# Performance work log

Measured on AMD Instinct MI355X. Metric: run time of the kernel, lower is better.

## Reference

```python
import jax, jax.numpy as jnp
import numpy as np

B, S, F, H, W = 16, 2048, 512, 512, 5
PAD = W // 2


def setup_inputs() -> dict:
    key = jax.random.key(0)
    k = jax.random.split(key, 6)
    scale = 0.02
    return {
        "embeds_output": jax.random.normal(k[0], (B, S, F), dtype=jnp.float32),
        "Wq": jax.random.normal(k[1], (F, H), dtype=jnp.float32) * scale,
        "Wk": jax.random.normal(k[2], (F, H), dtype=jnp.float32) * scale,
        "v_att": jax.random.normal(k[3], (H,), dtype=jnp.float32) * scale,
        "cnn_W": jax.random.normal(k[4], (W * F, H), dtype=jnp.float32) * scale,
        "cnn_b": jax.random.normal(k[5], (H,), dtype=jnp.float32) * scale,
    }


def reference(embeds_output, Wq, Wk, v_att, cnn_W, cnn_b):
    b, s, f = embeds_output.shape
    # getConvEmbeds: zero-pad and gather W shifted views -> [B, S, W, F]
    xp = jnp.pad(embeds_output, ((0, 0), (PAD, PAD), (0, 0)))
    windows = jnp.stack([xp[:, i:i + s, :] for i in range(W)], axis=2)  # [B,S,W,F]
    entity = windows[:, :, PAD, :]  # center token, [B,S,F]
    # Bahdanau additive attention over the window
    q = jnp.einsum('bsf,fh->bsh', entity, Wq)          # [B,S,H]
    kproj = jnp.einsum('bswf,fh->bswh', windows, Wk)   # [B,S,W,H]
    scores = jnp.einsum('bswh,h->bsw', jnp.tanh(kproj + q[:, :, None, :]), v_att)
    att = jax.nn.softmax(scores, axis=-1)              # [B,S,W]
    # weight contexts, flatten window dim (row-major W*F, matching torch reshape)
    att_context = (att[..., None] * windows).reshape(b, s, W * F)
    return att_context @ cnn_W + cnn_b                 # [B,S,H]
```

## Files before the change

kernel.cpp:

```cpp
#include <hip/hip_runtime.h>
#include <stdint.h>
#include <stddef.h>

typedef unsigned short u16;
typedef __attribute__((ext_vector_type(8))) short s16x8;
typedef __attribute__((ext_vector_type(8))) unsigned short u16x8;
typedef __attribute__((ext_vector_type(4))) unsigned short u16x4;
typedef __attribute__((ext_vector_type(4))) float f32x4;

typedef __attribute__((address_space(3))) void* as3_void_p;
typedef const __attribute__((address_space(1))) void* as1_cvoid_p;

#define GLD16(gp, lp) __builtin_amdgcn_global_load_lds((as1_cvoid_p)(gp), (as3_void_p)(lp), 16, 0, 0)

enum {
  NS = 2048, NF = 512, NH = 512, NW = 5,
  NROW = 32768,
  K2 = NW * NF,
  XBLOCKS = NROW * NF / 4 / 256,
  W_ELEMS = 1024 * 512 + 512 * K2,
  WBLOCKS = (W_ELEMS + 255) / 256
};

__device__ __forceinline__ u16 f2bf(float f) {
  unsigned u = __float_as_uint(f);
  u += 0x7FFFu + ((u >> 16) & 1u);
  return (u16)(u >> 16);
}
__device__ __forceinline__ float bf2f(u16 v) {
  return __uint_as_float(((unsigned)v) << 16);
}


__global__ __launch_bounds__(256) void cvt_all(const float* __restrict__ X,
                                               const float* __restrict__ Wq,
                                               const float* __restrict__ Wk,
                                               const float* __restrict__ cnnW,
                                               u16* __restrict__ Xb,
                                               u16* __restrict__ Wt1,
                                               u16* __restrict__ Wt2) {
  int b = blockIdx.x;
  if (b < XBLOCKS) {
    int i = b * 256 + threadIdx.x;
    f32x4 v = ((const f32x4*)X)[i];
    u16x4 o;
    o.x = f2bf(v.x); o.y = f2bf(v.y); o.z = f2bf(v.z); o.w = f2bf(v.w);
    ((u16x4*)Xb)[i] = o;
  } else {
    int i = (b - XBLOCKS) * 256 + threadIdx.x;
    if (i >= W_ELEMS) return;
    if (i < 1024 * 512) {
      int j = i >> 9, f = i & 511;
      float v = (j < 512) ? Wq[(size_t)f * 512 + j] : Wk[(size_t)f * 512 + (j - 512)];
      Wt1[i] = f2bf(v);
    } else {
      int t = i - 1024 * 512;
      int h = t / K2, k = t % K2;
      Wt2[t] = f2bf(cnnW[(size_t)k * 512 + h]);
    }
  }
}


__global__ __launch_bounds__(512, 4) void gemm_qk(const u16* __restrict__ Xb,
                                                  const u16* __restrict__ Wt1,
                                                  u16* __restrict__ QKb) {
  __shared__ u16 As[128 * 64];
  __shared__ u16 Bs[128 * 64];
  const int tid  = threadIdx.x;
  const int lane = tid & 63, wid = tid >> 6;
  const int wr = wid >> 2, wc = wid & 3;
  const int fr = lane & 15, fq = lane >> 4;
  const int wgid = (blockIdx.x & 7) * 256 + (blockIdx.x >> 3);
  const int brow = (wgid >> 3) * 128;
  const int bcol = (wgid & 7) * 128;

  const int rsub = tid >> 3;
  const int cb   = (((tid & 7) ^ (rsub & 7)) << 4);
  const char* gA0 = (const char*)(Xb  + (size_t)(brow + rsub) * NF) + cb;
  const char* gA1 = (const char*)(Xb  + (size_t)(brow + 64 + rsub) * NF) + cb;
  const char* gB0 = (const char*)(Wt1 + (size_t)(bcol + rsub) * NF) + cb;
  const char* gB1 = (const char*)(Wt1 + (size_t)(bcol + 64 + rsub) * NF) + cb;

  f32x4 acc[4][2] = {};

  for (int kt = 0; kt < 8; ++kt) {
    const int ko = kt * 128;
    GLD16(gA0 + ko, (char*)As + tid * 16);
    GLD16(gA1 + ko, (char*)As + 8192 + tid * 16);
    GLD16(gB0 + ko, (char*)Bs + tid * 16);
    GLD16(gB1 + ko, (char*)Bs + 8192 + tid * 16);
    __syncthreads();
#pragma unroll
    for (int kk = 0; kk < 2; ++kk) {
      s16x8 af[4], bfr[2];
#pragma unroll
      for (int m = 0; m < 4; ++m) {
        int row = wr * 64 + m * 16 + fr;
        af[m] = *(const s16x8*)((const char*)As + row * 128 + ((kk * 64 + fq * 16) ^ ((row & 7) << 4)));
      }
#pragma unroll
      for (int n = 0; n < 2; ++n) {
        int row = wc * 32 + n * 16 + fr;
        bfr[n] = *(const s16x8*)((const char*)Bs + row * 128 + ((kk * 64 + fq * 16) ^ ((row & 7) << 4)));
      }
#pragma unroll
      for (int m = 0; m < 4; ++m)
#pragma unroll
        for (int n = 0; n < 2; ++n)
          acc[m][n] = __builtin_amdgcn_mfma_f32_16x16x32_bf16(af[m], bfr[n], acc[m][n], 0, 0, 0);
    }
    __syncthreads();
  }

#pragma unroll
  for (int m = 0; m < 4; ++m)
#pragma unroll
    for (int n = 0; n < 2; ++n)
#pragma unroll
      for (int r = 0; r < 4; ++r) {
        int row = brow + wr * 64 + m * 16 + fq * 4 + r;
        int col = bcol + wc * 32 + n * 16 + fr;
        QKb[(size_t)row * 1024 + col] = f2bf(acc[m][n][r]);
      }
}


__global__ __launch_bounds__(256) void scores_att(const u16* __restrict__ QKb,
                                                  const float* __restrict__ vatt,
                                                  float* __restrict__ att) {
  const int lane = threadIdx.x & 63;
  const int wid  = threadIdx.x >> 6;
  const int wgid = (blockIdx.x & 7) * 1024 + (blockIdx.x >> 3);
  const int n = wgid * 4 + wid;
  const int s = n & (NS - 1);
  const int h0 = lane * 8;

  u16x8 qv = *(const u16x8*)(QKb + (size_t)n * 1024 + h0);
  f32x4 va0 = *(const f32x4*)(vatt + h0);
  f32x4 va1 = *(const f32x4*)(vatt + h0 + 4);
  float q[8], vv[8];
#pragma unroll
  for (int j = 0; j < 8; ++j) q[j] = bf2f(qv[j]);
  vv[0] = va0.x; vv[1] = va0.y; vv[2] = va0.z; vv[3] = va0.w;
  vv[4] = va1.x; vv[5] = va1.y; vv[6] = va1.z; vv[7] = va1.w;

  float sc[5];
#pragma unroll
  for (int w = 0; w < 5; ++w) {
    int sp = s + w - 2;
    u16x8 kv = {0, 0, 0, 0, 0, 0, 0, 0};
    if (sp >= 0 && sp < NS)
      kv = *(const u16x8*)(QKb + (size_t)(n + w - 2) * 1024 + 512 + h0);
    float acc = 0.f;
#pragma unroll
    for (int j = 0; j < 8; ++j) {
      float x = q[j] + bf2f(kv[j]);
      x = fminf(fmaxf(x, -15.f), 15.f);
      float e = __expf(2.f * x);
      acc += vv[j] * ((e - 1.f) / (e + 1.f));
    }
    sc[w] = acc;
  }
#pragma unroll
  for (int w = 0; w < 5; ++w)
#pragma unroll
    for (int o = 32; o > 0; o >>= 1)
      sc[w] += __shfl_xor(sc[w], o, 64);

  if (lane == 0) {
    float m = sc[0];
#pragma unroll
    for (int w = 1; w < 5; ++w) m = fmaxf(m, sc[w]);
    float e[5], sum = 0.f;
#pragma unroll
    for (int w = 0; w < 5; ++w) { e[w] = __expf(sc[w] - m); sum += e[w]; }
    float inv = 1.f / sum;
#pragma unroll
    for (int w = 0; w < 5; ++w) att[(size_t)n * 5 + w] = e[w] * inv;
  }
}


__global__ __launch_bounds__(512, 4) void gemm_out(const u16* __restrict__ Xb,
                                                   const u16* __restrict__ Wt2,
                                                   const float* __restrict__ att,
                                                   const float* __restrict__ cnnb,
                                                   float* __restrict__ out) {
  __shared__ u16 As[128 * 64];
  __shared__ u16 Bs[128 * 64];
  __shared__ float att_s[128 * 5];
  const int tid  = threadIdx.x;
  const int lane = tid & 63, wid = tid >> 6;
  const int wr = wid >> 2, wc = wid & 3;
  const int fr = lane & 15, fq = lane >> 4;
  const int wgid = (blockIdx.x & 7) * 128 + (blockIdx.x >> 3);
  const int brow = (wgid >> 2) * 128;
  const int bcol = (wgid & 3) * 128;

  if (tid < 128) {
    int s = (brow + tid) & (NS - 1);
#pragma unroll
    for (int w = 0; w < 5; ++w) {
      int sp = s + w - 2;
      att_s[tid * 5 + w] = (sp >= 0 && sp < NS) ? att[(size_t)(brow + tid) * 5 + w] : 0.f;
    }
  }

  const int rsub = tid >> 3;
  const int cb   = (((tid & 7) ^ (rsub & 7)) << 4);
  const char* gB0 = (const char*)(Wt2 + (size_t)(bcol + rsub) * K2) + cb;
  const char* gB1 = (const char*)(Wt2 + (size_t)(bcol + 64 + rsub) * K2) + cb;

  f32x4 acc[4][2] = {};
  f32x4 accOut[4][2] = {};

  for (int w = 0; w < 5; ++w) {
    int g0 = brow + rsub + w - 2;
    int g1 = brow + 64 + rsub + w - 2;
    g0 = g0 < 0 ? 0 : (g0 >= NROW ? NROW - 1 : g0);
    g1 = g1 < 0 ? 0 : (g1 >= NROW ? NROW - 1 : g1);
    const char* gA0 = (const char*)(Xb + (size_t)g0 * NF) + cb;
    const char* gA1 = (const char*)(Xb + (size_t)g1 * NF) + cb;
    const char* gBw0 = gB0 + w * 1024;
    const char* gBw1 = gB1 + w * 1024;

    for (int kt = 0; kt < 8; ++kt) {
      const int ko = kt * 128;
      GLD16(gA0  + ko, (char*)As + tid * 16);
      GLD16(gA1  + ko, (char*)As + 8192 + tid * 16);
      GLD16(gBw0 + ko, (char*)Bs + tid * 16);
      GLD16(gBw1 + ko, (char*)Bs + 8192 + tid * 16);
      __syncthreads();
#pragma unroll
      for (int kk = 0; kk < 2; ++kk) {
        s16x8 af[4], bfr[2];
#pragma unroll
        for (int m = 0; m < 4; ++m) {
          int row = wr * 64 + m * 16 + fr;
          af[m] = *(const s16x8*)((const char*)As + row * 128 + ((kk * 64 + fq * 16) ^ ((row & 7) << 4)));
        }
#pragma unroll
        for (int n = 0; n < 2; ++n) {
          int row = wc * 32 + n * 16 + fr;
          bfr[n] = *(const s16x8*)((const char*)Bs + row * 128 + ((kk * 64 + fq * 16) ^ ((row & 7) << 4)));
        }
#pragma unroll
        for (int m = 0; m < 4; ++m)
#pragma unroll
          for (int n = 0; n < 2; ++n)
            acc[m][n] = __builtin_amdgcn_mfma_f32_16x16x32_bf16(af[m], bfr[n], acc[m][n], 0, 0, 0);
      }
      __syncthreads();
    }
#pragma unroll
    for (int m = 0; m < 4; ++m) {
      float a0 = att_s[(wr * 64 + m * 16 + fq * 4 + 0) * 5 + w];
      float a1 = att_s[(wr * 64 + m * 16 + fq * 4 + 1) * 5 + w];
      float a2 = att_s[(wr * 64 + m * 16 + fq * 4 + 2) * 5 + w];
      float a3 = att_s[(wr * 64 + m * 16 + fq * 4 + 3) * 5 + w];
#pragma unroll
      for (int n = 0; n < 2; ++n) {
        accOut[m][n][0] += a0 * acc[m][n][0];
        accOut[m][n][1] += a1 * acc[m][n][1];
        accOut[m][n][2] += a2 * acc[m][n][2];
        accOut[m][n][3] += a3 * acc[m][n][3];
        acc[m][n] = f32x4{0.f, 0.f, 0.f, 0.f};
      }
    }
  }

#pragma unroll
  for (int m = 0; m < 4; ++m)
#pragma unroll
    for (int n = 0; n < 2; ++n)
#pragma unroll
      for (int r = 0; r < 4; ++r) {
        int row = brow + wr * 64 + m * 16 + fq * 4 + r;
        int col = bcol + wc * 32 + n * 16 + fr;
        out[(size_t)row * NH + col] = accOut[m][n][r] + cnnb[col];
      }
}


extern "C" void kernel_launch(void* const* d_in, const int* in_sizes, int n_in,
                              void* d_out, int out_size, void* d_ws, size_t ws_size,
                              hipStream_t stream) {
  const float* X    = (const float*)d_in[0];
  const float* Wq   = (const float*)d_in[1];
  const float* Wk   = (const float*)d_in[2];
  const float* vatt = (const float*)d_in[3];
  const float* cnnW = (const float*)d_in[4];
  const float* cnnb = (const float*)d_in[5];
  float* out = (float*)d_out;

  char* ws = (char*)d_ws;
  u16*   Xb  = (u16*)ws;
  u16*   Wt1 = (u16*)(ws + 33554432);
  u16*   Wt2 = (u16*)(ws + 34603008);
  u16*   QKb = (u16*)(ws + 37224448);
  float* att = (float*)(ws + 104333312);

  cvt_all<<<dim3(XBLOCKS + WBLOCKS), dim3(256), 0, stream>>>(X, Wq, Wk, cnnW, Xb, Wt1, Wt2);
  gemm_qk<<<dim3(2048), dim3(512), 0, stream>>>(Xb, Wt1, QKb);
  scores_att<<<dim3(NROW / 4), dim3(256), 0, stream>>>(QKb, vatt, att);
  gemm_out<<<dim3(1024), dim3(512), 0, stream>>>(Xb, Wt2, att, cnnb, out);
}
```

Before: 202.0 us.

## Double-buffer LDS tiles in gemm_out to overlap global loads with MFMA

Splits the A and B shared-memory tiles into two buffers and prefetches the next K-tile, or the first tile of the next window shift, with global_load_lds while the current tile feeds the MFMAs. Partial waits on vmcnt and raw s_barrier replace the full __syncthreads pairs, so load latency is meant to hide behind compute. LDS use doubles to about 64KB per block, which may lower occupancy under launch_bounds(512,4). The vmcnt counting is hand-managed, so it is fragile if the compiler emits other vector memory operations.

```diff
diff --git a/kernel.cpp b/kernel.cpp
--- a/kernel.cpp
+++ b/kernel.cpp
@@ -187,8 +187,8 @@
                                                    const float* __restrict__ att,
                                                    const float* __restrict__ cnnb,
                                                    float* __restrict__ out) {
-  __shared__ u16 As[128 * 64];
-  __shared__ u16 Bs[128 * 64];
+  __shared__ u16 As[2][128 * 64];
+  __shared__ u16 Bs[2][128 * 64];
   __shared__ float att_s[128 * 5];
   const int tid  = threadIdx.x;
   const int lane = tid & 63, wid = tid >> 6;
@@ -212,62 +212,98 @@
   const char* gB0 = (const char*)(Wt2 + (size_t)(bcol + rsub) * K2) + cb;
   const char* gB1 = (const char*)(Wt2 + (size_t)(bcol + 64 + rsub) * K2) + cb;
 
+  auto abase = [&](int w, int add64) -> const char* {
+    int g = brow + add64 + rsub + w - 2;
+    g = g < 0 ? 0 : (g >= NROW ? NROW - 1 : g);
+    return (const char*)(Xb + (size_t)g * NF) + cb;
+  };
+
   f32x4 acc[4][2] = {};
   f32x4 accOut[4][2] = {};
 
+  const char* gA0 = abase(0, 0);
+  const char* gA1 = abase(0, 64);
+
+  GLD16(gA0, (char*)As[0] + tid * 16);
+  GLD16(gA1, (char*)As[0] + 8192 + tid * 16);
+  GLD16(gB0, (char*)Bs[0] + tid * 16);
+  GLD16(gB1, (char*)Bs[0] + 8192 + tid * 16);
+  __syncthreads();
+
+  int cur = 0;
   for (int w = 0; w < 5; ++w) {
-    int g0 = brow + rsub + w - 2;
-    int g1 = brow + 64 + rsub + w - 2;
-    g0 = g0 < 0 ? 0 : (g0 >= NROW ? NROW - 1 : g0);
-    g1 = g1 < 0 ? 0 : (g1 >= NROW ? NROW - 1 : g1);
-    const char* gA0 = (const char*)(Xb + (size_t)g0 * NF) + cb;
-    const char* gA1 = (const char*)(Xb + (size_t)g1 * NF) + cb;
     const char* gBw0 = gB0 + w * 1024;
     const char* gBw1 = gB1 + w * 1024;
+    const char* nA0 = (w < 4) ? abase(w + 1, 0)  : gA0;
+    const char* nA1 = (w < 4) ? abase(w + 1, 64) : gA1;
 
     for (int kt = 0; kt < 8; ++kt) {
-      const int ko = kt * 128;
-      GLD16(gA0  + ko, (char*)As + tid * 16);
-      GLD16(gA1  + ko, (char*)As + 8192 + tid * 16);
-      GLD16(gBw0 + ko, (char*)Bs + tid * 16);
-      GLD16(gBw1 + ko, (char*)Bs + 8192 + tid * 16);
-      __syncthreads();
+      const bool last = (w == 4) && (kt == 7);
+      const int nb = cur ^ 1;
+      if (!last) {
+        if (kt < 7) {
+          const int ko = (kt + 1) * 128;
+          GLD16(gA0  + ko, (char*)As[nb] + tid * 16);
+          GLD16(gA1  + ko, (char*)As[nb] + 8192 + tid * 16);
+          GLD16(gBw0 + ko, (char*)Bs[nb] + tid * 16);
+          GLD16(gBw1 + ko, (char*)Bs[nb] + 8192 + tid * 16);
+        } else {
+          GLD16(nA0,         (char*)As[nb] + tid * 16);
+          GLD16(nA1,         (char*)As[nb] + 8192 + tid * 16);
+          GLD16(gBw0 + 1024, (char*)Bs[nb] + tid * 16);
+          GLD16(gBw1 + 1024, (char*)Bs[nb] + 8192 + tid * 16);
+        }
+        asm volatile("s_waitcnt vmcnt(4)" ::: "memory");
+      } else {
+        asm volatile("s_waitcnt vmcnt(0)" ::: "memory");
+      }
+      __builtin_amdgcn_s_barrier();
+
+      const char* Ab = (const char*)As[cur];
+      const char* Bb = (const char*)Bs[cur];
 #pragma unroll
       for (int kk = 0; kk < 2; ++kk) {
         s16x8 af[4], bfr[2];
 #pragma unroll
         for (int m = 0; m < 4; ++m) {
           int row = wr * 64 + m * 16 + fr;
-          af[m] = *(const s16x8*)((const char*)As + row * 128 + ((kk * 64 + fq * 16) ^ ((row & 7) << 4)));
+          af[m] = *(const s16x8*)(Ab + row * 128 + ((kk * 64 + fq * 16) ^ ((row & 7) << 4)));
         }
 #pragma unroll
         for (int n = 0; n < 2; ++n) {
           int row = wc * 32 + n * 16 + fr;
-          bfr[n] = *(const s16x8*)((const char*)Bs + row * 128 + ((kk * 64 + fq * 16) ^ ((row & 7) << 4)));
+          bfr[n] = *(const s16x8*)(Bb + row * 128 + ((kk * 64 + fq * 16) ^ ((row & 7) << 4)));
         }
+        asm volatile("s_waitcnt lgkmcnt(0)" ::: "memory");
+        __builtin_amdgcn_sched_barrier(0);
 #pragma unroll
         for (int m = 0; m < 4; ++m)
 #pragma unroll
           for (int n = 0; n < 2; ++n)
             acc[m][n] = __builtin_amdgcn_mfma_f32_16x16x32_bf16(af[m], bfr[n], acc[m][n], 0, 0, 0);
       }
-      __syncthreads();
-    }
-#pragma unroll
-    for (int m = 0; m < 4; ++m) {
-      float a0 = att_s[(wr * 64 + m * 16 + fq * 4 + 0) * 5 + w];
-      float a1 = att_s[(wr * 64 + m * 16 + fq * 4 + 1) * 5 + w];
-      float a2 = att_s[(wr * 64 + m * 16 + fq * 4 + 2) * 5 + w];
-      float a3 = att_s[(wr * 64 + m * 16 + fq * 4 + 3) * 5 + w];
-#pragma unroll
-      for (int n = 0; n < 2; ++n) {
-        accOut[m][n][0] += a0 * acc[m][n][0];
-        accOut[m][n][1] += a1 * acc[m][n][1];
-        accOut[m][n][2] += a2 * acc[m][n][2];
-        accOut[m][n][3] += a3 * acc[m][n][3];
-        acc[m][n] = f32x4{0.f, 0.f, 0.f, 0.f};
-      }
-    }
+      if (kt == 7) {
+#pragma unroll
+        for (int m = 0; m < 4; ++m) {
+          float a0 = att_s[(wr * 64 + m * 16 + fq * 4 + 0) * 5 + w];
+          float a1 = att_s[(wr * 64 + m * 16 + fq * 4 + 1) * 5 + w];
+          float a2 = att_s[(wr * 64 + m * 16 + fq * 4 + 2) * 5 + w];
+          float a3 = att_s[(wr * 64 + m * 16 + fq * 4 + 3) * 5 + w];
+#pragma unroll
+          for (int n = 0; n < 2; ++n) {
+            accOut[m][n][0] += a0 * acc[m][n][0];
+            accOut[m][n][1] += a1 * acc[m][n][1];
+            accOut[m][n][2] += a2 * acc[m][n][2];
+            accOut[m][n][3] += a3 * acc[m][n][3];
+            acc[m][n] = f32x4{0.f, 0.f, 0.f, 0.f};
+          }
+        }
+      }
+      __builtin_amdgcn_s_barrier();
+      cur ^= 1;
+    }
+    gA0 = nA0;
+    gA1 = nA1;
   }
 
 #pragma unroll
```

New measurement: 201.0 us. Within noise of the previous version (-0.5%).

## Triple-buffer LDS with async prefetch and enlarge GEMM row tiles to 256

Applied to the files above, without the earlier changes.

Both bf16 GEMMs move from single-buffered LDS with two syncthreads per K step to a three-slot ring buffer. Global-to-LDS loads are issued two stages ahead and gated by vmcnt waits plus one barrier per iteration. The output tile grows to 256 rows, which doubles A reuse per B fragment, and gemm_out flattens its window and K loops into one 40-step pipeline. The cost is more LDS (about 144KB per block), more accumulator registers, occupancy lowered to 2 blocks, and half as many blocks in the grid.

```diff
diff --git a/kernel.cpp b/kernel.cpp
--- a/kernel.cpp
+++ b/kernel.cpp
@@ -62,64 +62,82 @@
 }
 
 
-__global__ __launch_bounds__(512, 4) void gemm_qk(const u16* __restrict__ Xb,
+__global__ __launch_bounds__(512, 2) void gemm_qk(const u16* __restrict__ Xb,
                                                   const u16* __restrict__ Wt1,
                                                   u16* __restrict__ QKb) {
-  __shared__ u16 As[128 * 64];
-  __shared__ u16 Bs[128 * 64];
+  __shared__ u16 As[3][256 * 64];
+  __shared__ u16 Bs[3][128 * 64];
   const int tid  = threadIdx.x;
   const int lane = tid & 63, wid = tid >> 6;
   const int wr = wid >> 2, wc = wid & 3;
   const int fr = lane & 15, fq = lane >> 4;
-  const int wgid = (blockIdx.x & 7) * 256 + (blockIdx.x >> 3);
-  const int brow = (wgid >> 3) * 128;
+  const int wgid = (blockIdx.x & 7) * 128 + (blockIdx.x >> 3);
+  const int brow = (wgid >> 3) * 256;
   const int bcol = (wgid & 7) * 128;
 
   const int rsub = tid >> 3;
-  const int cb   = (((tid & 7) ^ (rsub & 7)) << 4);
-  const char* gA0 = (const char*)(Xb  + (size_t)(brow + rsub) * NF) + cb;
-  const char* gA1 = (const char*)(Xb  + (size_t)(brow + 64 + rsub) * NF) + cb;
-  const char* gB0 = (const char*)(Wt1 + (size_t)(bcol + rsub) * NF) + cb;
-  const char* gB1 = (const char*)(Wt1 + (size_t)(bcol + 64 + rsub) * NF) + cb;
-
-  f32x4 acc[4][2] = {};
-
-  for (int kt = 0; kt < 8; ++kt) {
-    const int ko = kt * 128;
-    GLD16(gA0 + ko, (char*)As + tid * 16);
-    GLD16(gA1 + ko, (char*)As + 8192 + tid * 16);
-    GLD16(gB0 + ko, (char*)Bs + tid * 16);
-    GLD16(gB1 + ko, (char*)Bs + 8192 + tid * 16);
-    __syncthreads();
+  const int cbyte = (((tid & 7) ^ (rsub & 7)) << 4);
+  const char* gA[4];
+  const char* gB[2];
+#pragma unroll
+  for (int g = 0; g < 4; ++g)
+    gA[g] = (const char*)(Xb + (size_t)(brow + g * 64 + rsub) * NF) + cbyte;
+#pragma unroll
+  for (int g = 0; g < 2; ++g)
+    gB[g] = (const char*)(Wt1 + (size_t)(bcol + g * 64 + rsub) * NF) + cbyte;
+
+  f32x4 acc[8][2] = {};
+
+  auto STAGE = [&](int s, int slot) {
+    const int ko = s * 128;
+    char* ab = (char*)&As[slot][0];
+    char* bb = (char*)&Bs[slot][0];
+#pragma unroll
+    for (int g = 0; g < 4; ++g) GLD16(gA[g] + ko, ab + g * 8192 + tid * 16);
+#pragma unroll
+    for (int g = 0; g < 2; ++g) GLD16(gB[g] + ko, bb + g * 8192 + tid * 16);
+  };
+
+  STAGE(0, 0);
+  STAGE(1, 1);
+
+  int rd = 0;
+  for (int it = 0; it < 8; ++it) {
+    if (it < 7) asm volatile("s_waitcnt vmcnt(6)" ::: "memory");
+    else        asm volatile("s_waitcnt vmcnt(0)" ::: "memory");
+    __builtin_amdgcn_s_barrier();
+    if (it + 2 < 8) {
+      int st = rd + 2; if (st >= 3) st -= 3;
+      STAGE(it + 2, st);
+    }
+    const char* Ab = (const char*)&As[rd][0];
+    const char* Bb = (const char*)&Bs[rd][0];
 #pragma unroll
     for (int kk = 0; kk < 2; ++kk) {
-      s16x8 af[4], bfr[2];
-#pragma unroll
-      for (int m = 0; m < 4; ++m) {
-        int row = wr * 64 + m * 16 + fr;
-        af[m] = *(const s16x8*)((const char*)As + row * 128 + ((kk * 64 + fq * 16) ^ ((row & 7) << 4)));
-      }
+      s16x8 bfr[2];
 #pragma unroll
       for (int n = 0; n < 2; ++n) {
         int row = wc * 32 + n * 16 + fr;
-        bfr[n] = *(const s16x8*)((const char*)Bs + row * 128 + ((kk * 64 + fq * 16) ^ ((row & 7) << 4)));
-      }
-#pragma unroll
-      for (int m = 0; m < 4; ++m)
-#pragma unroll
-        for (int n = 0; n < 2; ++n)
-          acc[m][n] = __builtin_amdgcn_mfma_f32_16x16x32_bf16(af[m], bfr[n], acc[m][n], 0, 0, 0);
-    }
-    __syncthreads();
-  }
-
-#pragma unroll
-  for (int m = 0; m < 4; ++m)
+        bfr[n] = *(const s16x8*)(Bb + row * 128 + ((kk * 64 + fq * 16) ^ ((row & 7) << 4)));
+      }
+#pragma unroll
+      for (int m = 0; m < 8; ++m) {
+        int row = wr * 128 + m * 16 + fr;
+        s16x8 af = *(const s16x8*)(Ab + row * 128 + ((kk * 64 + fq * 16) ^ ((row & 7) << 4)));
+        acc[m][0] = __builtin_amdgcn_mfma_f32_16x16x32_bf16(af, bfr[0], acc[m][0], 0, 0, 0);
+        acc[m][1] = __builtin_amdgcn_mfma_f32_16x16x32_bf16(af, bfr[1], acc[m][1], 0, 0, 0);
+      }
+    }
+    rd = rd + 1; if (rd >= 3) rd = 0;
+  }
+
+#pragma unroll
+  for (int m = 0; m < 8; ++m)
 #pragma unroll
     for (int n = 0; n < 2; ++n)
 #pragma unroll
       for (int r = 0; r < 4; ++r) {
-        int row = brow + wr * 64 + m * 16 + fq * 4 + r;
+        int row = brow + wr * 128 + m * 16 + fq * 4 + r;
         int col = bcol + wc * 32 + n * 16 + fr;
         QKb[(size_t)row * 1024 + col] = f2bf(acc[m][n][r]);
       }
@@ -182,23 +200,23 @@
 }
 
 
-__global__ __launch_bounds__(512, 4) void gemm_out(const u16* __restrict__ Xb,
+__global__ __launch_bounds__(512, 2) void gemm_out(const u16* __restrict__ Xb,
                                                    const u16* __restrict__ Wt2,
                                                    const float* __restrict__ att,
                                                    const float* __restrict__ cnnb,
                                                    float* __restrict__ out) {
-  __shared__ u16 As[128 * 64];
-  __shared__ u16 Bs[128 * 64];
-  __shared__ float att_s[128 * 5];
+  __shared__ u16 As[3][256 * 64];
+  __shared__ u16 Bs[3][128 * 64];
+  __shared__ float att_s[256 * 5];
   const int tid  = threadIdx.x;
   const int lane = tid & 63, wid = tid >> 6;
   const int wr = wid >> 2, wc = wid & 3;
   const int fr = lane & 15, fq = lane >> 4;
-  const int wgid = (blockIdx.x & 7) * 128 + (blockIdx.x >> 3);
-  const int brow = (wgid >> 2) * 128;
+  const int wgid = (blockIdx.x & 7) * 64 + (blockIdx.x >> 3);
+  const int brow = (wgid >> 2) * 256;
   const int bcol = (wgid & 3) * 128;
 
-  if (tid < 128) {
+  if (tid < 256) {
     int s = (brow + tid) & (NS - 1);
 #pragma unroll
     for (int w = 0; w < 5; ++w) {
@@ -208,75 +226,99 @@
   }
 
   const int rsub = tid >> 3;
-  const int cb   = (((tid & 7) ^ (rsub & 7)) << 4);
-  const char* gB0 = (const char*)(Wt2 + (size_t)(bcol + rsub) * K2) + cb;
-  const char* gB1 = (const char*)(Wt2 + (size_t)(bcol + 64 + rsub) * K2) + cb;
-
-  f32x4 acc[4][2] = {};
-  f32x4 accOut[4][2] = {};
-
-  for (int w = 0; w < 5; ++w) {
-    int g0 = brow + rsub + w - 2;
-    int g1 = brow + 64 + rsub + w - 2;
-    g0 = g0 < 0 ? 0 : (g0 >= NROW ? NROW - 1 : g0);
-    g1 = g1 < 0 ? 0 : (g1 >= NROW ? NROW - 1 : g1);
-    const char* gA0 = (const char*)(Xb + (size_t)g0 * NF) + cb;
-    const char* gA1 = (const char*)(Xb + (size_t)g1 * NF) + cb;
-    const char* gBw0 = gB0 + w * 1024;
-    const char* gBw1 = gB1 + w * 1024;
-
-    for (int kt = 0; kt < 8; ++kt) {
-      const int ko = kt * 128;
-      GLD16(gA0  + ko, (char*)As + tid * 16);
-      GLD16(gA1  + ko, (char*)As + 8192 + tid * 16);
-      GLD16(gBw0 + ko, (char*)Bs + tid * 16);
-      GLD16(gBw1 + ko, (char*)Bs + 8192 + tid * 16);
-      __syncthreads();
-#pragma unroll
-      for (int kk = 0; kk < 2; ++kk) {
-        s16x8 af[4], bfr[2];
-#pragma unroll
-        for (int m = 0; m < 4; ++m) {
-          int row = wr * 64 + m * 16 + fr;
-          af[m] = *(const s16x8*)((const char*)As + row * 128 + ((kk * 64 + fq * 16) ^ ((row & 7) << 4)));
+  const int cbyte = (((tid & 7) ^ (rsub & 7)) << 4);
+  const char* gB[2];
+#pragma unroll
+  for (int g = 0; g < 2; ++g)
+    gB[g] = (const char*)(Wt2 + (size_t)(bcol + g * 64 + rsub) * K2) + cbyte;
+
+  const char* gA[4];
+  auto setA = [&](int w) {
+#pragma unroll
+    for (int g = 0; g < 4; ++g) {
+      int r = brow + g * 64 + rsub + w - 2;
+      r = r < 0 ? 0 : (r >= NROW ? NROW - 1 : r);
+      gA[g] = (const char*)(Xb + (size_t)r * NF) + cbyte;
+    }
+  };
+
+  auto STAGE = [&](int s, int slot) {
+    const int ka = (s & 7) * 128;
+    const int kb = s * 128;
+    char* ab = (char*)&As[slot][0];
+    char* bb = (char*)&Bs[slot][0];
+#pragma unroll
+    for (int g = 0; g < 4; ++g) GLD16(gA[g] + ka, ab + g * 8192 + tid * 16);
+#pragma unroll
+    for (int g = 0; g < 2; ++g) GLD16(gB[g] + kb, bb + g * 8192 + tid * 16);
+  };
+
+  f32x4 acc[8][2] = {};
+  f32x4 accOut[8][2] = {};
+
+  setA(0);
+  STAGE(0, 0);
+  STAGE(1, 1);
+
+  int rd = 0;
+  for (int it = 0; it < 40; ++it) {
+    if (it < 39) asm volatile("s_waitcnt vmcnt(6)" ::: "memory");
+    else         asm volatile("s_waitcnt vmcnt(0)" ::: "memory");
+    __builtin_amdgcn_s_barrier();
+    {
+      int s = it + 2;
+      if (s < 40) {
+        if ((s & 7) == 0) setA(s >> 3);
+        int st = rd + 2; if (st >= 3) st -= 3;
+        STAGE(s, st);
+      }
+    }
+    const char* Ab = (const char*)&As[rd][0];
+    const char* Bb = (const char*)&Bs[rd][0];
+#pragma unroll
+    for (int kk = 0; kk < 2; ++kk) {
+      s16x8 bfr[2];
+#pragma unroll
+      for (int n = 0; n < 2; ++n) {
+        int row = wc * 32 + n * 16 + fr;
+        bfr[n] = *(const s16x8*)(Bb + row * 128 + ((kk * 64 + fq * 16) ^ ((row & 7) << 4)));
+      }
+#pragma unroll
+      for (int m = 0; m < 8; ++m) {
+        int row = wr * 128 + m * 16 + fr;
+        s16x8 af = *(const s16x8*)(Ab + row * 128 + ((kk * 64 + fq * 16) ^ ((row & 7) << 4)));
+        acc[m][0] = __builtin_amdgcn_mfma_f32_16x16x32_bf16(af, bfr[0], acc[m][0], 0, 0, 0);
+        acc[m][1] = __builtin_amdgcn_mfma_f32_16x16x32_bf16(af, bfr[1], acc[m][1], 0, 0, 0);
+      }
+    }
+    if ((it & 7) == 7) {
+      int w = it >> 3;
+#pragma unroll
+      for (int m = 0; m < 8; ++m) {
+        float a0 = att_s[(wr * 128 + m * 16 + fq * 4 + 0) * 5 + w];
+        float a1 = att_s[(wr * 128 + m * 16 + fq * 4 + 1) * 5 + w];
+        float a2 = att_s[(wr * 128 + m * 16 + fq * 4 + 2) * 5 + w];
+        float a3 = att_s[(wr * 128 + m * 16 + fq * 4 + 3) * 5 + w];
+#pragma unroll
+        for (int n = 0; n < 2; ++n) {
+          accOut[m][n][0] += a0 * acc[m][n][0];
+          accOut[m][n][1] += a1 * acc[m][n][1];
+          accOut[m][n][2] += a2 * acc[m][n][2];
+          accOut[m][n][3] += a3 * acc[m][n][3];
+          acc[m][n] = f32x4{0.f, 0.f, 0.f, 0.f};
         }
-#pragma unroll
-        for (int n = 0; n < 2; ++n) {
-          int row = wc * 32 + n * 16 + fr;
-          bfr[n] = *(const s16x8*)((const char*)Bs + row * 128 + ((kk * 64 + fq * 16) ^ ((row & 7) << 4)));
-        }
-#pragma unroll
-        for (int m = 0; m < 4; ++m)
-#pragma unroll
-          for (int n = 0; n < 2; ++n)
-            acc[m][n] = __builtin_amdgcn_mfma_f32_16x16x32_bf16(af[m], bfr[n], acc[m][n], 0, 0, 0);
-      }
-      __syncthreads();
-    }
-#pragma unroll
-    for (int m = 0; m < 4; ++m) {
-      float a0 = att_s[(wr * 64 + m * 16 + fq * 4 + 0) * 5 + w];
-      float a1 = att_s[(wr * 64 + m * 16 + fq * 4 + 1) * 5 + w];
-      float a2 = att_s[(wr * 64 + m * 16 + fq * 4 + 2) * 5 + w];
-      float a3 = att_s[(wr * 64 + m * 16 + fq * 4 + 3) * 5 + w];
-#pragma unroll
-      for (int n = 0; n < 2; ++n) {
-        accOut[m][n][0] += a0 * acc[m][n][0];
-        accOut[m][n][1] += a1 * acc[m][n][1];
-        accOut[m][n][2] += a2 * acc[m][n][2];
-        accOut[m][n][3] += a3 * acc[m][n][3];
-        acc[m][n] = f32x4{0.f, 0.f, 0.f, 0.f};
-      }
-    }
-  }
-
-#pragma unroll
-  for (int m = 0; m < 4; ++m)
+      }
+    }
+    rd = rd + 1; if (rd >= 3) rd = 0;
+  }
+
+#pragma unroll
+  for (int m = 0; m < 8; ++m)
 #pragma unroll
     for (int n = 0; n < 2; ++n)
 #pragma unroll
       for (int r = 0; r < 4; ++r) {
-        int row = brow + wr * 64 + m * 16 + fq * 4 + r;
+        int row = brow + wr * 128 + m * 16 + fq * 4 + r;
         int col = bcol + wc * 32 + n * 16 + fr;
         out[(size_t)row * NH + col] = accOut[m][n][r] + cnnb[col];
       }
@@ -302,7 +344,7 @@
   float* att = (float*)(ws + 104333312);
 
   cvt_all<<<dim3(XBLOCKS + WBLOCKS), dim3(256), 0, stream>>>(X, Wq, Wk, cnnW, Xb, Wt1, Wt2);
-  gemm_qk<<<dim3(2048), dim3(512), 0, stream>>>(Xb, Wt1, QKb);
+  gemm_qk<<<dim3(1024), dim3(512), 0, stream>>>(Xb, Wt1, QKb);
   scores_att<<<dim3(NROW / 4), dim3(256), 0, stream>>>(QKb, vatt, att);
-  gemm_out<<<dim3(1024), dim3(512), 0, stream>>>(Xb, Wt2, att, cnnb, out);
-}
+  gemm_out<<<dim3(512), dim3(512), 0, stream>>>(Xb, Wt2, att, cnnb, out);
+}
```

Result: slower. 243.2 us (+20.4%).
